# Kernel tuning notes

Measured on AMD Instinct MI355X. Metric: run time of the kernel, lower is better.

## Reference

```python
import jax, jax.numpy as jnp
import numpy as np

N_STEPS = 2048  # forward arg `n`: number of recurrence steps


def setup_inputs() -> dict:
    key = jax.random.key(0)
    kx, k2, k3, kb, k4 = jax.random.split(key, 5)
    x = jax.random.normal(kx, (5,), dtype=jnp.float32)
    # scalar weights of the 1x1 Linears; kept small so the 2047-step
    # recurrence (factor 1 - w2^2 - w4^2) stays numerically stable
    w2 = jax.random.uniform(k2, (), jnp.float32, -0.3, 0.3)  # lambda2.weight
    w3 = jax.random.uniform(k3, (), jnp.float32, -0.3, 0.3)  # lambda3.weight
    b3 = jax.random.uniform(kb, (), jnp.float32, -0.3, 0.3)  # lambda3.bias
    w4 = jax.random.uniform(k4, (), jnp.float32, -0.3, 0.3)  # lambda4.weight
    return {"x": x, "w2": w2, "w3": w3, "b3": b3, "w4": w4, "n": N_STEPS}


def reference(x, w2, w3, b3, w4, n):
    # Faithful SIR recurrence. In the torch module, ns[i] starts as zeros(5)
    # and only slots 0..3 are written, so slot 4 is 0 for every step i >= 1.
    x = x.reshape(5)

    def step(s, _):
        s0, s1, s2, s3 = s[0], s[1], s[2], s[3]
        a = w2 * (w2 * s0)                              # lambda2(lambda2(s0))
        b = w4 * (w4 * s0)                              # lambda4(lambda4(s0))
        c = w3 * (w3 * (s0 / 1000.0 * s2) + b3) + b3    # lambda3(lambda3(s0/1000*s2))
        new = jnp.stack([s0 - a - b + c, s1 + a, s2 - c, s3 + b,
                         jnp.zeros_like(s0)])
        return new, new

    _, ys = jax.lax.scan(step, x, None, length=n - 1)
    return ys  # (n-1, 5): rows ns[1]..ns[n-1] concatenated, as in torch
```

## Files before the change

### kernel.cpp

```cpp
#include <hip/hip_runtime.h>


typedef float f2 __attribute__((ext_vector_type(2)));

template <int CTRL, int RMASK>
__device__ __forceinline__ float dpp0(float x) {
  return __int_as_float(__builtin_amdgcn_update_dpp(
      0, __float_as_int(x), CTRL, RMASK, 0xf, false));
}

__device__ __forceinline__ float wave_incl_scan(float x) {
  x += dpp0<0x111, 0xf>(x);
  x += dpp0<0x112, 0xf>(x);
  x += dpp0<0x114, 0xf>(x);
  x += dpp0<0x118, 0xf>(x);
  x += dpp0<0x142, 0xa>(x);
  x += dpp0<0x143, 0xc>(x);
  return x;
}

__global__ __launch_bounds__(64) void sir_kernel(
    const float* __restrict__ x, const float* __restrict__ w2p,
    const float* __restrict__ w3p, const float* __restrict__ b3p,
    const float* __restrict__ w4p, const int* __restrict__ np,
    float* __restrict__ out) {
  const int lane = threadIdx.x;
  const int n = *np;
  const int rows = n - 1;

  const float w2 = *w2p, w3 = *w3p, b3 = *b3p, w4 = *w4p;
  const float w2sq   = w2 * w2;
  const float w4sq   = w4 * w4;
  const float L      = 1.0f - w2sq - w4sq;
  const float gamma  = (w3 * w3) / 1000.0f;
  const float delta  = fmaf(w3, b3, b3);

  const float s1_0 = x[1], s3_0 = x[3];

  if (rows == 2047) {
    f2 W;  W.x = x[0];  W.y = x[2];
    f2 C1; C1.x = gamma; C1.y = -gamma;
    f2 C2; C2.x = L;     C2.y = 1.0f;
    f2 C3; C3.x = delta; C3.y = -delta;

    float G = W.x;
    float puA = 0.f, pvA = 0.f, puB = 0.f, pvB = 0.f;
    float* __restrict__ o = out + 5 * lane;

#define SIR_BLOCK(PU, PV, LAST)                                          \
  {                                                                      \
    _Pragma("unroll")                                                    \
    for (int j = 0; j < 64; ++j) {                                       \
      f2 FG;                                                             \
      asm("v_pk_fma_f32 %0, %1, %2, %3 op_sel:[0,1,0] op_sel_hi:[1,0,1]" \
          : "=v"(FG)                                                     \
          : "v"(C1), "v"(W), "v"(C2));        \
      asm("v_pk_fma_f32 %0, %0, %1, %2"                                  \
          : "+v"(W)                                                      \
          : "v"(FG), "v"(C3));                 \
      const bool park = (lane == j);                                     \
      PU = park ? W.x : PU;                                              \
      PV = park ? W.y : PV;                                              \
    }                                                                    \
    const float S   = wave_incl_scan(PU);                                \
    const float T   = (G + S) - PU;              \
    const float s1v = fmaf(w2sq, T, s1_0);                               \
    const float s3v = fmaf(w4sq, T, s3_0);                               \
    G += __shfl(S, 63);                                                  \
    if (!(LAST) || lane < 63) {              \
      o[0] = PU; o[1] = s1v; o[2] = PV; o[3] = s3v; o[4] = 0.0f;         \
    }                                                                    \
    o += 5 * 64;                                                         \
  }

#pragma unroll 1
    for (int bb = 0; bb < 16; ++bb) {
      SIR_BLOCK(puA, pvA, false)
      SIR_BLOCK(puB, pvB, bb == 15)
    }
#undef SIR_BLOCK
  } else {
    if (lane == 0) {
      float u = x[0], v = x[2], s1 = s1_0, s3 = s3_0;
      const float mgamma = -gamma, mdelta = -delta;
      float* __restrict__ p = out;
#pragma unroll 4
      for (int i = 0; i < rows; ++i) {
        const float f = fmaf(gamma, v, L);
        const float g = fmaf(mgamma, u, 1.0f);
        s1 = fmaf(w2sq, u, s1);
        s3 = fmaf(w4sq, u, s3);
        u = fmaf(u, f, delta);
        v = fmaf(v, g, mdelta);
        p[0] = u; p[1] = s1; p[2] = v; p[3] = s3; p[4] = 0.0f;
        p += 5;
      }
    }
  }
}

extern "C" void kernel_launch(void* const* d_in, const int* in_sizes, int n_in,
                              void* d_out, int out_size, void* d_ws, size_t ws_size,
                              hipStream_t stream) {
  const float* x   = (const float*)d_in[0];
  const float* w2  = (const float*)d_in[1];
  const float* w3  = (const float*)d_in[2];
  const float* b3  = (const float*)d_in[3];
  const float* w4  = (const float*)d_in[4];
  const int*   n   = (const int*)d_in[5];
  float* out = (float*)d_out;
  sir_kernel<<<1, 64, 0, stream>>>(x, w2, w3, b3, w4, n, out);
}
```

Baseline: 91.63 us.

## Park state every 8 steps and recompute rows per lane in parallel

The serial wave-wide recurrence now records a lane's state only every 8th step, instead of running a select on every step. After each 512-step block, each lane replays 7 further steps from its parked state to rebuild its 8 rows. A single scan over the per-lane 8-row sums then forms the cumulative s1/s3 terms, replacing 32 scans with 4. Each lane writes its contiguous 40-float span with float4 stores. The aim is to shorten the per-step critical-path instruction count and cut scan and store overhead, at the cost of more registers and a small amount of redundant recompute.

```diff
diff --git a/kernel.cpp b/kernel.cpp
--- a/kernel.cpp
+++ b/kernel.cpp
@@ -2,6 +2,11 @@
 
 
 typedef float f2 __attribute__((ext_vector_type(2)));
+
+#define STEP(Wv, FGv)                                                    \
+  asm("v_pk_fma_f32 %0, %1, %2, %3 op_sel:[0,1,0] op_sel_hi:[1,0,1]"     \
+      : "=v"(FGv) : "v"(C1), "v"(Wv), "v"(C2));                          \
+  asm("v_pk_fma_f32 %0, %0, %1, %2" : "+v"(Wv) : "v"(FGv), "v"(C3));
 
 template <int CTRL, int RMASK>
 __device__ __forceinline__ float dpp0(float x) {
@@ -29,12 +34,11 @@
   const int rows = n - 1;
 
   const float w2 = *w2p, w3 = *w3p, b3 = *b3p, w4 = *w4p;
-  const float w2sq   = w2 * w2;
-  const float w4sq   = w4 * w4;
-  const float L      = 1.0f - w2sq - w4sq;
-  const float gamma  = (w3 * w3) / 1000.0f;
-  const float delta  = fmaf(w3, b3, b3);
-
+  const float w2sq  = w2 * w2;
+  const float w4sq  = w4 * w4;
+  const float L     = 1.0f - w2sq - w4sq;
+  const float gamma = (w3 * w3) / 1000.0f;
+  const float delta = fmaf(w3, b3, b3);
   const float s1_0 = x[1], s3_0 = x[3];
 
   if (rows == 2047) {
@@ -44,41 +48,54 @@
     f2 C3; C3.x = delta; C3.y = -delta;
 
     float G = W.x;
-    float puA = 0.f, pvA = 0.f, puB = 0.f, pvB = 0.f;
-    float* __restrict__ o = out + 5 * lane;
-
-#define SIR_BLOCK(PU, PV, LAST)                                          \
-  {                                                                      \
-    _Pragma("unroll")                                                    \
-    for (int j = 0; j < 64; ++j) {                                       \
-      f2 FG;                                                             \
-      asm("v_pk_fma_f32 %0, %1, %2, %3 op_sel:[0,1,0] op_sel_hi:[1,0,1]" \
-          : "=v"(FG)                                                     \
-          : "v"(C1), "v"(W), "v"(C2));        \
-      asm("v_pk_fma_f32 %0, %0, %1, %2"                                  \
-          : "+v"(W)                                                      \
-          : "v"(FG), "v"(C3));                 \
-      const bool park = (lane == j);                                     \
-      PU = park ? W.x : PU;                                              \
-      PV = park ? W.y : PV;                                              \
-    }                                                                    \
-    const float S   = wave_incl_scan(PU);                                \
-    const float T   = (G + S) - PU;              \
-    const float s1v = fmaf(w2sq, T, s1_0);                               \
-    const float s3v = fmaf(w4sq, T, s3_0);                               \
-    G += __shfl(S, 63);                                                  \
-    if (!(LAST) || lane < 63) {              \
-      o[0] = PU; o[1] = s1v; o[2] = PV; o[3] = s3v; o[4] = 0.0f;         \
-    }                                                                    \
-    o += 5 * 64;                                                         \
-  }
 
 #pragma unroll 1
-    for (int bb = 0; bb < 16; ++bb) {
-      SIR_BLOCK(puA, pvA, false)
-      SIR_BLOCK(puB, pvB, bb == 15)
+    for (int b = 0; b < 4; ++b) {
+      float PU = 0.0f, PV = 0.0f;
+#pragma unroll
+      for (int jj = 0; jj < 64; ++jj) {
+        f2 FG;
+        STEP(W, FG)
+        const bool park = (lane == jj);
+        PU = park ? W.x : PU;
+        PV = park ? W.y : PV;
+#pragma unroll
+        for (int t = 1; t < 8; ++t) { f2 FG2; STEP(W, FG2) }
+      }
+      float U[8], V[8];
+      f2 R; R.x = PU; R.y = PV;
+      U[0] = PU; V[0] = PV;
+#pragma unroll
+      for (int t = 1; t < 8; ++t) { f2 FG; STEP(R, FG) U[t] = R.x; V[t] = R.y; }
+      float Q = U[0];
+#pragma unroll
+      for (int t = 1; t < 8; ++t) Q += U[t];
+      const float S = wave_incl_scan(Q);
+      float T = G + (S - Q);
+      G += __shfl(S, 63);
+      float flat[40];
+#pragma unroll
+      for (int t = 0; t < 8; ++t) {
+        flat[5 * t + 0] = U[t];
+        flat[5 * t + 1] = fmaf(w2sq, T, s1_0);
+        flat[5 * t + 2] = V[t];
+        flat[5 * t + 3] = fmaf(w4sq, T, s3_0);
+        flat[5 * t + 4] = 0.0f;
+        T += U[t];
+      }
+      float4* __restrict__ q4 = (float4*)(out + 2560 * b + 40 * lane);
+      if (b < 3 || lane < 63) {
+#pragma unroll
+        for (int k = 0; k < 10; ++k)
+          q4[k] = make_float4(flat[4*k], flat[4*k+1], flat[4*k+2], flat[4*k+3]);
+      } else {
+#pragma unroll
+        for (int k = 0; k < 8; ++k)
+          q4[k] = make_float4(flat[4*k], flat[4*k+1], flat[4*k+2], flat[4*k+3]);
+        ((float2*)(q4 + 8))[0] = make_float2(flat[32], flat[33]);
+        ((float*)q4)[34] = flat[34];
+      }
     }
-#undef SIR_BLOCK
   } else {
     if (lane == 0) {
       float u = x[0], v = x[2], s1 = s1_0, s3 = s3_0;
```

Result: faster. 80.09 us (-12.6%).
